# Kernel tuning notes

Hardware: AMD Instinct MI355X
Metric: run time of the kernel (lower is better)

## Reference

```python
import jax, jax.numpy as jnp
import numpy as np

NUM_EMBEDDINGS = 4096
EMBEDDING_DIM = 256
COMMITMENT_COST = 0.25
DECAY = 0.99
EPS = 1e-5
NORM_EPS = 1e-6
B, T = 64, 1024


def _l2norm(x):
    # torch.nn.functional.normalize: x / max(||x||_2, eps)
    n = jnp.sqrt(jnp.sum(x * x, axis=-1, keepdims=True))
    return x / jnp.maximum(n, NORM_EPS)


def setup_inputs() -> dict:
    key = jax.random.key(0)
    k1, k2 = jax.random.split(key)
    z = jax.random.normal(k1, (B, EMBEDDING_DIM, T), dtype=jnp.float32)
    weight = jax.random.normal(k2, (NUM_EMBEDDINGS, EMBEDDING_DIM), dtype=jnp.float32)
    weight = weight.at[0].set(0.0)  # reserved zero code
    ema_cluster_size = jnp.zeros((NUM_EMBEDDINGS,), dtype=jnp.float32)
    ema_w = weight  # buffer initialized as a clone of the codebook
    return {"z": z, "weight": weight, "ema_cluster_size": ema_cluster_size, "ema_w": ema_w}


def reference(z, weight, ema_cluster_size, ema_w):
    K = weight.shape[0]
    zp = jnp.transpose(z, (0, 2, 1))            # [B, T, D]
    b, t, d = zp.shape
    flat_z = zp.reshape(-1, d)                  # [N, D]
    flat_z_norm = _l2norm(flat_z)
    weight_norm = _l2norm(weight)
    # cosine similarity; argmin(1 - cos) == argmax(cos); code 0 excluded via -inf
    cos_sim = jnp.einsum('nd,kd->nk', flat_z_norm, weight_norm)
    cos_sim = cos_sim.at[:, 0].set(-jnp.inf)
    idx = jnp.argmax(cos_sim, axis=1)           # [N] int
    q = weight[idx].reshape(zp.shape)           # [B, T, D]

    # --- training-mode EMA codebook update (buffer math, no grad) ---
    counts = jax.ops.segment_sum(jnp.ones_like(idx, dtype=flat_z.dtype), idx, num_segments=K)
    new_cs = DECAY * ema_cluster_size + (1.0 - DECAY) * counts
    dw = jax.ops.segment_sum(flat_z_norm, idx, num_segments=K)  # [K, D]
    new_ema_w = DECAY * ema_w + (1.0 - DECAY) * dw
    new_cs = new_cs.at[0].set(0.0)
    new_ema_w = new_ema_w.at[0].set(0.0)
    n = jnp.sum(new_cs)
    cluster_size = (new_cs + EPS) / (n + K * EPS) * n
    new_weight = _l2norm(new_ema_w / cluster_size[:, None])
    new_weight = new_weight.at[0].set(0.0)

    loss = COMMITMENT_COST * jnp.mean((jax.lax.stop_gradient(q) - zp) ** 2)
    quantized = zp + jax.lax.stop_gradient(q - zp)  # straight-through
    quantized = jnp.transpose(quantized, (0, 2, 1))  # back to [B, D, T]
    codes = idx.reshape(b, t)
    return quantized, loss, codes, new_weight, new_cs, new_ema_w
```

## Files before the change

kernel.cpp:

```cpp
#include <hip/hip_runtime.h>
#include <math.h>

#define NUM_K 4096
#define DIM   256
#define TLEN  1024
#define DT    (DIM * TLEN)
#define CAP   2048

typedef short bf16x8 __attribute__((ext_vector_type(8)));
typedef float f32x4  __attribute__((ext_vector_type(4)));

static __device__ __forceinline__ unsigned short f2bf(float x) {
  unsigned u = __float_as_uint(x);
  u += 0x7fffu + ((u >> 16) & 1u);
  return (unsigned short)(u >> 16);
}

static __device__ __forceinline__ f32x4 mfma16(bf16x8 a, bf16x8 b, f32x4 c) {
  return __builtin_amdgcn_mfma_f32_16x16x32_bf16(a, b, c, 0, 0, 0);
}

__global__ __launch_bounds__(256) void wnorm_kernel(const float* __restrict__ w,
                                                    float* __restrict__ wnorms) {
  const int k = blockIdx.x * 256 + threadIdx.x;
  const float* row = w + (size_t)k * DIM;
  float p[2];
#pragma unroll
  for (int blk = 0; blk < 2; ++blk) {
    const float* b = row + blk * 128;
    float r[8];
#pragma unroll
    for (int j = 0; j < 8; ++j) r[j] = __fmul_rn(b[j], b[j]);
    for (int i = 8; i < 128; i += 8) {
#pragma unroll
      for (int j = 0; j < 8; ++j) r[j] = __fadd_rn(r[j], __fmul_rn(b[i + j], b[i + j]));
    }
    p[blk] = __fadd_rn(__fadd_rn(__fadd_rn(r[0], r[1]), __fadd_rn(r[2], r[3])),
                       __fadd_rn(__fadd_rn(r[4], r[5]), __fadd_rn(r[6], r[7])));
  }
  wnorms[k] = fmaxf(__fsqrt_rn(__fadd_rn(p[0], p[1])), 1e-6f);
}

__global__ __launch_bounds__(256) void wfrag_kernel(const float* __restrict__ w,
                                                    const float* __restrict__ wnorms,
                                                    unsigned short* __restrict__ img) {
  const int t = blockIdx.x * 256 + threadIdx.x;
  const int lane = t & 63;
  const int fragid = t >> 6;
  const int jg = fragid & 3;
  const int kb = (fragid >> 2) & 7;
  const int chunk = fragid >> 5;
  const int c  = (chunk << 6) + (jg << 4) + (lane & 15);
  const int d0 = (kb << 5) + ((lane >> 4) << 3);
  const float m = wnorms[c];
  const float* src = w + (size_t)c * DIM + d0;
  union { bf16x8 v; unsigned short u[8]; } o;
#pragma unroll
  for (int u = 0; u < 8; ++u) o.u[u] = f2bf(__fdiv_rn(src[u], m));
  *reinterpret_cast<bf16x8*>(img + (size_t)fragid * 512 + lane * 8) = o.v;
}

__global__ __launch_bounds__(256, 3) void vq_main_kernel(
    const float* __restrict__ z, const float* __restrict__ weight,
    const unsigned short* __restrict__ wimg, const float* __restrict__ wnorms,
    float* __restrict__ znT, float* __restrict__ out_codes,
    float* __restrict__ counts, float* __restrict__ loss_accum) {
  __shared__ float tnorm[64];
  __shared__ float v1p[2][64];
  __shared__ float thr[64];
  __shared__ int   fidx[64];
  __shared__ int   clist[CAP];
  __shared__ float cscore[CAP];
  __shared__ int   ccount;

  const int tid  = threadIdx.x;
  const int bb   = blockIdx.x >> 4;
  const int t0   = (blockIdx.x & 15) << 6;
  const int lane = tid & 63;
  const int wv   = tid >> 6;
  const int wr   = wv >> 1;
  const int wc   = wv & 1;
  const float* zb = z + (size_t)bb * DT + t0;

  bf16x8 afr[2][8];
  {
    const int tloc = (wr << 5) + (lane & 15);
    const int dr   = (lane >> 4) << 3;
#pragma unroll
    for (int i = 0; i < 2; ++i) {
      const float* zc = zb + tloc + (i << 4);
#pragma unroll
      for (int kb = 0; kb < 8; ++kb) {
        union { bf16x8 v; unsigned short u[8]; } a;
#pragma unroll
        for (int u = 0; u < 8; ++u)
          a.u[u] = f2bf(zc[(size_t)((kb << 5) + dr + u) * TLEN]);
        afr[i][kb] = a.v;
      }
    }
  }

  if (tid < 64) {
    const float* zc = zb + tid;
    float p[2];
#pragma unroll
    for (int blk = 0; blk < 2; ++blk) {
      float r[8];
#pragma unroll
      for (int j = 0; j < 8; ++j) {
        const float v = zc[(size_t)(blk * 128 + j) * TLEN];
        r[j] = __fmul_rn(v, v);
      }
      for (int i = 8; i < 128; i += 8) {
#pragma unroll
        for (int j = 0; j < 8; ++j) {
          const float v = zc[(size_t)(blk * 128 + i + j) * TLEN];
          r[j] = __fadd_rn(r[j], __fmul_rn(v, v));
        }
      }
      p[blk] = __fadd_rn(__fadd_rn(__fadd_rn(r[0], r[1]), __fadd_rn(r[2], r[3])),
                         __fadd_rn(__fadd_rn(r[4], r[5]), __fadd_rn(r[6], r[7])));
    }
    tnorm[tid] = fmaxf(__fsqrt_rn(__fadd_rn(p[0], p[1])), 1e-6f);
  }
  if (tid == 0) ccount = 0;

  const unsigned short* bbase = wimg + (wc << 10) + (lane << 3);
  const f32x4 zero4 = {0.f, 0.f, 0.f, 0.f};

  float v1loc[2][4];
#pragma unroll
  for (int i = 0; i < 2; ++i)
#pragma unroll
    for (int r = 0; r < 4; ++r) v1loc[i][r] = -INFINITY;
  {
    const bool lc0 = (wc == 0) && ((lane & 15) == 0);
#pragma unroll 1
    for (int chunk = 0; chunk < 64; ++chunk) {
      const unsigned short* bc_ = bbase + ((size_t)chunk << 14);
      bf16x8 bf[16];
#pragma unroll
      for (int kb = 0; kb < 8; ++kb) {
        bf[kb]     = *reinterpret_cast<const bf16x8*>(bc_ + (kb << 11));
        bf[kb + 8] = *reinterpret_cast<const bf16x8*>(bc_ + (kb << 11) + 512);
      }
      f32x4 acc[2][2];
      acc[0][0] = zero4; acc[0][1] = zero4; acc[1][0] = zero4; acc[1][1] = zero4;
      __builtin_amdgcn_s_setprio(1);
#pragma unroll
      for (int kb = 0; kb < 8; ++kb) {
        acc[0][0] = mfma16(afr[0][kb], bf[kb],     acc[0][0]);
        acc[1][0] = mfma16(afr[1][kb], bf[kb],     acc[1][0]);
        acc[0][1] = mfma16(afr[0][kb], bf[kb + 8], acc[0][1]);
        acc[1][1] = mfma16(afr[1][kb], bf[kb + 8], acc[1][1]);
      }
      __builtin_amdgcn_s_setprio(0);
#pragma unroll
      for (int i = 0; i < 2; ++i)
#pragma unroll
        for (int r = 0; r < 4; ++r) {
          float v0 = acc[i][0][r];
          if (chunk == 0 && lc0) v0 = -INFINITY;
          v1loc[i][r] = fmaxf(v1loc[i][r], fmaxf(v0, acc[i][1][r]));
        }
    }
  }
#pragma unroll
  for (int i = 0; i < 2; ++i)
#pragma unroll
    for (int r = 0; r < 4; ++r) {
      float v = v1loc[i][r];
      v = fmaxf(v, __shfl_xor(v, 1));
      v = fmaxf(v, __shfl_xor(v, 2));
      v = fmaxf(v, __shfl_xor(v, 4));
      v = fmaxf(v, __shfl_xor(v, 8));
      if ((lane & 15) == 0)
        v1p[wc][(wr << 5) + (i << 4) + ((lane >> 4) << 2) + r] = v;
    }
  __syncthreads();
  if (tid < 64) thr[tid] = fmaxf(v1p[0][tid], v1p[1][tid]) - 0.02f * tnorm[tid];
  __syncthreads();

  float thrv_[2][4];
  {
    const int tb = (wr << 5) + ((lane >> 4) << 2);
#pragma unroll
    for (int i = 0; i < 2; ++i)
#pragma unroll
      for (int r = 0; r < 4; ++r) thrv_[i][r] = thr[tb + (i << 4) + r];
  }

  {
#pragma unroll 1
    for (int chunk = 0; chunk < 64; ++chunk) {
      const unsigned short* bc_ = bbase + ((size_t)chunk << 14);
      bf16x8 bf[16];
#pragma unroll
      for (int kb = 0; kb < 8; ++kb) {
        bf[kb]     = *reinterpret_cast<const bf16x8*>(bc_ + (kb << 11));
        bf[kb + 8] = *reinterpret_cast<const bf16x8*>(bc_ + (kb << 11) + 512);
      }
      f32x4 acc[2][2];
      acc[0][0] = zero4; acc[0][1] = zero4; acc[1][0] = zero4; acc[1][1] = zero4;
      __builtin_amdgcn_s_setprio(1);
#pragma unroll
      for (int kb = 0; kb < 8; ++kb) {
        acc[0][0] = mfma16(afr[0][kb], bf[kb],     acc[0][0]);
        acc[1][0] = mfma16(afr[1][kb], bf[kb],     acc[1][0]);
        acc[0][1] = mfma16(afr[0][kb], bf[kb + 8], acc[0][1]);
        acc[1][1] = mfma16(afr[1][kb], bf[kb + 8], acc[1][1]);
      }
      __builtin_amdgcn_s_setprio(0);
#pragma unroll
      for (int i = 0; i < 2; ++i)
#pragma unroll
        for (int j = 0; j < 2; ++j) {
          const int c = (chunk << 6) + (wc << 5) + (j << 4) + (lane & 15);
#pragma unroll
          for (int r = 0; r < 4; ++r) {
            if (acc[i][j][r] >= thrv_[i][r] && c != 0) {
              const int pos = atomicAdd(&ccount, 1);
              if (pos < CAP)
                clist[pos] = (c << 7) | ((wr << 5) + (i << 4) + ((lane >> 4) << 2) + r);
            }
          }
        }
    }
  }
  __syncthreads();

  const int ncand = min(ccount, CAP);
  for (int e = tid; e < ncand; e += 256) {
    const int pk = clist[e];
    const int tloc = pk & 127;
    const int c = pk >> 7;
    const float m  = tnorm[tloc];
    const float mc = wnorms[c];
    const float* zc = zb + tloc;
    const float* wp = weight + (size_t)c * DIM;
    float s = 0.f;
#pragma unroll 8
    for (int d = 0; d < DIM; ++d)
      s = fmaf(__fdiv_rn(zc[(size_t)d * TLEN], m), __fdiv_rn(wp[d], mc), s);
    cscore[e] = s;
  }
  __syncthreads();

  if (tid < 64) {
    float best = -INFINITY; int bc = NUM_K;
    for (int e = 0; e < ncand; ++e) {
      const int pk = clist[e];
      if ((pk & 127) == tid) {
        const float s = cscore[e]; const int c = pk >> 7;
        if (s > best || (s == best && c < bc)) { best = s; bc = c; }
      }
    }
    if (bc >= NUM_K) bc = 1;
    fidx[tid] = bc;
    out_codes[bb * TLEN + t0 + tid] = (float)bc;
    atomicAdd(&counts[bc], 1.0f);
  }
  __syncthreads();

  {
    const int gbase = (bb << 10) + t0;
    float lpart = 0.f;
#pragma unroll 4
    for (int r = 0; r < 16; ++r) {
      const int tk = (r << 2) + wv;
      const int code = fidx[tk];
      const float m = tnorm[tk];
      const float* zc = zb + tk;
      const float4 w4 = *reinterpret_cast<const float4*>(
          weight + (size_t)code * DIM + (lane << 2));
      float4 zr4;
      zr4.x = zc[(size_t)((lane << 2) + 0) * TLEN];
      zr4.y = zc[(size_t)((lane << 2) + 1) * TLEN];
      zr4.z = zc[(size_t)((lane << 2) + 2) * TLEN];
      zr4.w = zc[(size_t)((lane << 2) + 3) * TLEN];
      float4 zn4;
      zn4.x = __fdiv_rn(zr4.x, m);
      zn4.y = __fdiv_rn(zr4.y, m);
      zn4.z = __fdiv_rn(zr4.z, m);
      zn4.w = __fdiv_rn(zr4.w, m);
      *reinterpret_cast<float4*>(znT + (size_t)(gbase + tk) * DIM + (lane << 2)) = zn4;
      const float dx = w4.x - zr4.x, dy = w4.y - zr4.y;
      const float dz = w4.z - zr4.z, dw_ = w4.w - zr4.w;
      lpart = fmaf(dx, dx, lpart); lpart = fmaf(dy, dy, lpart);
      lpart = fmaf(dz, dz, lpart); lpart = fmaf(dw_, dw_, lpart);
    }
#pragma unroll
    for (int off = 32; off; off >>= 1) lpart += __shfl_down(lpart, off, 64);
    if (lane == 0) atomicAdd(loss_accum, lpart);
  }
}

__global__ __launch_bounds__(256) void finalize_cs_kernel(
    const float* __restrict__ counts, const float* __restrict__ ema_cs,
    float* __restrict__ out_ncs, float* __restrict__ ws_n,
    const float* __restrict__ loss_accum, float* __restrict__ out_loss,
    int* __restrict__ offsets) {
  __shared__ float redf[4];
  __shared__ int   redi[4];
  const int tid = threadIdx.x;
  const int lane = tid & 63, wv = tid >> 6;
  const int base = tid << 4;
  int cloc[16]; int csum = 0; float fsum = 0.f;
#pragma unroll
  for (int j = 0; j < 16; ++j) {
    const int k = base + j;
    const float cf = counts[k];
    const float v = (k == 0) ? 0.f : 0.99f * ema_cs[k] + 0.01f * cf;
    out_ncs[k] = v; fsum += v;
    cloc[j] = csum; csum += (int)cf;
  }
  int inc = csum;
#pragma unroll
  for (int off = 1; off < 64; off <<= 1) {
    const int t = __shfl_up(inc, off, 64);
    if (lane >= off) inc += t;
  }
  float fs = fsum;
#pragma unroll
  for (int off = 32; off; off >>= 1) fs += __shfl_down(fs, off, 64);
  if (lane == 63) redi[wv] = inc;
  if (lane == 0)  redf[wv] = fs;
  __syncthreads();
  int wbase = 0;
#pragma unroll
  for (int w = 0; w < 4; ++w) wbase += (w < wv) ? redi[w] : 0;
  const int tbase = wbase + inc - csum;
#pragma unroll
  for (int j = 0; j < 16; ++j) offsets[base + j] = tbase + cloc[j];
  if (tid == 0) {
    ws_n[0] = redf[0] + redf[1] + redf[2] + redf[3];
    out_loss[0] = 0.25f * loss_accum[0] / 16777216.0f;
  }
}

__global__ __launch_bounds__(256) void scatter_kernel(
    const float* __restrict__ codes, const int* __restrict__ offsets,
    int* __restrict__ cursor, int* __restrict__ bucket) {
  const int g = blockIdx.x * 256 + threadIdx.x;
  const int c = (int)codes[g];
  const int pos = atomicAdd(&cursor[c], 1);
  bucket[offsets[c] + pos] = g;
}

__global__ __launch_bounds__(256) void dw_kernel(
    const float* __restrict__ znT, const float* __restrict__ counts,
    const int* __restrict__ offsets, const int* __restrict__ bucket,
    float* __restrict__ dw) {
  const int c = blockIdx.x;
  const int cnt = (int)counts[c];
  const int off = offsets[c];
  const int tid = threadIdx.x;
  float acc = 0.f;
  for (int i = 0; i < cnt; ++i) {
    const int g = bucket[off + i];
    acc += znT[(size_t)g * DIM + tid];
  }
  dw[(size_t)c * DIM + tid] = acc;
}

__global__ __launch_bounds__(256) void finalize_w_kernel(
    const float* __restrict__ ema_w, const float* __restrict__ ncs,
    const float* __restrict__ ws_n, float* __restrict__ new_ema_w,
    float* __restrict__ new_weight) {
  const int wid  = threadIdx.x >> 6;
  const int lane = threadIdx.x & 63;
  const int k    = (blockIdx.x << 2) + wid;
  const float n  = ws_n[0];
  const float cs = (ncs[k] + 1e-5f) / (n + 4096.0f * 1e-5f) * n;
  const float* erow = ema_w + k * DIM;
  float* nrow = new_ema_w + k * DIM;
  float* wrow = new_weight + k * DIM;
  const int d0 = lane << 2;
  float u[4]; float ss = 0.f;
#pragma unroll
  for (int j = 0; j < 4; ++j) {
    const float dwv = nrow[d0 + j];
    const float val = (k == 0) ? 0.f : 0.99f * erow[d0 + j] + 0.01f * dwv;
    nrow[d0 + j] = val;
    const float uu = val / cs;
    u[j] = uu;
    ss = fmaf(uu, uu, ss);
  }
#pragma unroll
  for (int off = 32; off; off >>= 1) ss += __shfl_xor(ss, off, 64);
  const float m = fmaxf(sqrtf(ss), 1e-6f);
#pragma unroll
  for (int j = 0; j < 4; ++j) wrow[d0 + j] = u[j] / m;
}

__global__ __launch_bounds__(256) void qwrite_kernel(
    const float* __restrict__ codes, const float* __restrict__ weight,
    float* __restrict__ out_q) {
  const int bb = blockIdx.x >> 4;
  const int t0 = (blockIdx.x & 15) << 6;
  const int ln = threadIdx.x & 63, qv = threadIdx.x >> 6;
  const int code = (int)codes[bb * TLEN + t0 + ln];
  const float* wrow = weight + (size_t)code * DIM;
  float* qb = out_q + (size_t)bb * DT + t0 + ln;
#pragma unroll 4
  for (int dd = 0; dd < 64; ++dd) {
    const int d = (qv << 6) + dd;
    qb[(size_t)d * TLEN] = wrow[d];
  }
}

extern "C" void kernel_launch(void* const* d_in, const int* in_sizes, int n_in,
                              void* d_out, int out_size, void* d_ws, size_t ws_size,
                              hipStream_t stream) {
  const float* z      = (const float*)d_in[0];
  const float* weight = (const float*)d_in[1];
  const float* ema_cs = (const float*)d_in[2];
  const float* ema_w  = (const float*)d_in[3];

  float* out = (float*)d_out;
  float* out_q     = out;
  float* out_loss  = out + 16777216;
  float* out_codes = out + 16777217;
  float* out_nw    = out + 16842753;
  float* out_ncs   = out + 17891329;
  float* out_new   = out + 17895425;

  float* counts     = (float*)d_ws;
  float* loss_accum = counts + 4096;
  float* ws_n       = counts + 4097;
  float* wnorms     = counts + 4352;

  unsigned short* wimg = (unsigned short*)(out_nw + 3);
  int* bucket  = (int*)(out_nw + 3);
  int* offsets = (int*)(out_nw + 524292);
  int* cursor  = (int*)(out_nw + 528388);

  hipMemsetAsync(d_ws, 0, 4098 * sizeof(float), stream);
  hipMemsetAsync(cursor, 0, 4096 * sizeof(int), stream);

  wnorm_kernel<<<16, 256, 0, stream>>>(weight, wnorms);
  wfrag_kernel<<<512, 256, 0, stream>>>(weight, wnorms, wimg);
  vq_main_kernel<<<1024, 256, 0, stream>>>(z, weight, wimg, wnorms, out_q ,
                                           out_codes, counts, loss_accum);
  finalize_cs_kernel<<<1, 256, 0, stream>>>(counts, ema_cs, out_ncs, ws_n,
                                            loss_accum, out_loss, offsets);
  scatter_kernel<<<256, 256, 0, stream>>>(out_codes, offsets, cursor, bucket);
  dw_kernel<<<NUM_K, 256, 0, stream>>>(out_q , counts, offsets, bucket, out_new);
  finalize_w_kernel<<<NUM_K / 4, 256, 0, stream>>>(ema_w, out_ncs, ws_n,
                                                   out_new, out_nw);
  qwrite_kernel<<<1024, 256, 0, stream>>>(out_codes, weight, out_q);
}
```

Before: 864.4 us.

## Double-buffer codebook fragment loads and precompute normalized vectors for rescoring

Both MFMA passes over the codebook now double-buffer the B fragments, loading the next chunk while the current one is multiplied, with sched barriers and a min-occupancy launch bound lowered from 3 to 2 to make room for the extra registers. Normalized z rows are written up front, and a separate kernel writes fp32 normalized codebook rows into the output scratch area. The candidate rescoring loop then reads those precomputed vectors instead of doing strided loads and two divisions per element. The costs are lower occupancy, an extra kernel launch and extra global traffic for the normalized weights.

New measurement: 759.8 us. 12.1% less time.

```diff
diff --git a/kernel.cpp b/kernel.cpp
--- a/kernel.cpp
+++ b/kernel.cpp
@@ -41,8 +41,19 @@
   wnorms[k] = fmaxf(__fsqrt_rn(__fadd_rn(p[0], p[1])), 1e-6f);
 }
 
-__global__ __launch_bounds__(256) void wfrag_kernel(const float* __restrict__ w,
+__global__ __launch_bounds__(256) void wnf32_kernel(const float* __restrict__ w,
                                                     const float* __restrict__ wnorms,
+                                                    float* __restrict__ wnf) {
+  const int idx = blockIdx.x * 256 + threadIdx.x;
+  const float m = wnorms[idx >> 6];
+  const float4 v = *reinterpret_cast<const float4*>(w + (size_t)idx * 4);
+  float4 o;
+  o.x = __fdiv_rn(v.x, m); o.y = __fdiv_rn(v.y, m);
+  o.z = __fdiv_rn(v.z, m); o.w = __fdiv_rn(v.w, m);
+  *reinterpret_cast<float4*>(wnf + (size_t)idx * 4) = o;
+}
+
+__global__ __launch_bounds__(256) void wfrag_kernel(const float* __restrict__ wnf,
                                                     unsigned short* __restrict__ img) {
   const int t = blockIdx.x * 256 + threadIdx.x;
   const int lane = t & 63;
@@ -52,19 +63,19 @@
   const int chunk = fragid >> 5;
   const int c  = (chunk << 6) + (jg << 4) + (lane & 15);
   const int d0 = (kb << 5) + ((lane >> 4) << 3);
-  const float m = wnorms[c];
-  const float* src = w + (size_t)c * DIM + d0;
+  const float* src = wnf + (size_t)c * DIM + d0;
   union { bf16x8 v; unsigned short u[8]; } o;
 #pragma unroll
-  for (int u = 0; u < 8; ++u) o.u[u] = f2bf(__fdiv_rn(src[u], m));
+  for (int u = 0; u < 8; ++u) o.u[u] = f2bf(src[u]);
   *reinterpret_cast<bf16x8*>(img + (size_t)fragid * 512 + lane * 8) = o.v;
 }
 
-__global__ __launch_bounds__(256, 3) void vq_main_kernel(
+__global__ __launch_bounds__(256, 2) void vq_main_kernel(
     const float* __restrict__ z, const float* __restrict__ weight,
-    const unsigned short* __restrict__ wimg, const float* __restrict__ wnorms,
+    const unsigned short* __restrict__ wimg, const float* __restrict__ wnf32,
     float* __restrict__ znT, float* __restrict__ out_codes,
     float* __restrict__ counts, float* __restrict__ loss_accum) {
+  __shared__ float pp[2][64];
   __shared__ float tnorm[64];
   __shared__ float v1p[2][64];
   __shared__ float thr[64];
@@ -82,6 +93,46 @@
   const int wc   = wv & 1;
   const float* zb = z + (size_t)bb * DT + t0;
 
+  if (tid < 128) {
+    const int tok = tid & 63, blk = tid >> 6;
+    const float* zc = zb + tok;
+    float r[8];
+#pragma unroll
+    for (int j = 0; j < 8; ++j) {
+      const float v = zc[(size_t)(blk * 128 + j) * TLEN];
+      r[j] = __fmul_rn(v, v);
+    }
+    for (int i = 8; i < 128; i += 8) {
+#pragma unroll
+      for (int j = 0; j < 8; ++j) {
+        const float v = zc[(size_t)(blk * 128 + i + j) * TLEN];
+        r[j] = __fadd_rn(r[j], __fmul_rn(v, v));
+      }
+    }
+    pp[blk][tok] = __fadd_rn(__fadd_rn(__fadd_rn(r[0], r[1]), __fadd_rn(r[2], r[3])),
+                             __fadd_rn(__fadd_rn(r[4], r[5]), __fadd_rn(r[6], r[7])));
+  }
+  if (tid == 0) ccount = 0;
+  __syncthreads();
+  if (tid < 64) tnorm[tid] = fmaxf(__fsqrt_rn(__fadd_rn(pp[0][tid], pp[1][tid])), 1e-6f);
+  __syncthreads();
+
+  {
+    const int tok = tid & 63, seg = tid >> 6;
+    const float m = tnorm[tok];
+    const float* zc = zb + tok;
+    float* orow = znT + (size_t)((bb << 10) + t0 + tok) * DIM + (seg << 6);
+#pragma unroll 4
+    for (int k4 = 0; k4 < 16; ++k4) {
+      float4 o;
+      o.x = __fdiv_rn(zc[(size_t)((seg << 6) + (k4 << 2) + 0) * TLEN], m);
+      o.y = __fdiv_rn(zc[(size_t)((seg << 6) + (k4 << 2) + 1) * TLEN], m);
+      o.z = __fdiv_rn(zc[(size_t)((seg << 6) + (k4 << 2) + 2) * TLEN], m);
+      o.w = __fdiv_rn(zc[(size_t)((seg << 6) + (k4 << 2) + 3) * TLEN], m);
+      *reinterpret_cast<float4*>(&orow[k4 << 2]) = o;
+    }
+  }
+
   bf16x8 afr[2][8];
   {
     const int tloc = (wr << 5) + (lane & 15);
@@ -100,33 +151,31 @@
     }
   }
 
-  if (tid < 64) {
-    const float* zc = zb + tid;
-    float p[2];
-#pragma unroll
-    for (int blk = 0; blk < 2; ++blk) {
-      float r[8];
-#pragma unroll
-      for (int j = 0; j < 8; ++j) {
-        const float v = zc[(size_t)(blk * 128 + j) * TLEN];
-        r[j] = __fmul_rn(v, v);
-      }
-      for (int i = 8; i < 128; i += 8) {
-#pragma unroll
-        for (int j = 0; j < 8; ++j) {
-          const float v = zc[(size_t)(blk * 128 + i + j) * TLEN];
-          r[j] = __fadd_rn(r[j], __fmul_rn(v, v));
-        }
-      }
-      p[blk] = __fadd_rn(__fadd_rn(__fadd_rn(r[0], r[1]), __fadd_rn(r[2], r[3])),
-                         __fadd_rn(__fadd_rn(r[4], r[5]), __fadd_rn(r[6], r[7])));
-    }
-    tnorm[tid] = fmaxf(__fsqrt_rn(__fadd_rn(p[0], p[1])), 1e-6f);
-  }
-  if (tid == 0) ccount = 0;
-
   const unsigned short* bbase = wimg + (wc << 10) + (lane << 3);
   const f32x4 zero4 = {0.f, 0.f, 0.f, 0.f};
+  const bool lc0 = (wc == 0) && ((lane & 15) == 0);
+
+#define LOADC(buf, ch) do {                                              \
+    const unsigned short* p_ = bbase + ((size_t)(ch) << 14);             \
+    _Pragma("unroll")                                                    \
+    for (int kb_ = 0; kb_ < 8; ++kb_) {                                  \
+      buf[kb_]     = *reinterpret_cast<const bf16x8*>(p_ + (kb_ << 11)); \
+      buf[kb_ + 8] = *reinterpret_cast<const bf16x8*>(p_ + (kb_ << 11) + 512); \
+    }                                                                    \
+    __builtin_amdgcn_sched_barrier(0);                                   \
+  } while (0)
+
+#define MFMAC(buf, accv) do {                                            \
+    __builtin_amdgcn_s_setprio(1);                                       \
+    _Pragma("unroll")                                                    \
+    for (int kb_ = 0; kb_ < 8; ++kb_) {                                  \
+      accv[0][0] = mfma16(afr[0][kb_], buf[kb_],     accv[0][0]);        \
+      accv[1][0] = mfma16(afr[1][kb_], buf[kb_],     accv[1][0]);        \
+      accv[0][1] = mfma16(afr[0][kb_], buf[kb_ + 8], accv[0][1]);        \
+      accv[1][1] = mfma16(afr[1][kb_], buf[kb_ + 8], accv[1][1]);        \
+    }                                                                    \
+    __builtin_amdgcn_s_setprio(0);                                       \
+  } while (0)
 
   float v1loc[2][4];
 #pragma unroll
@@ -134,35 +183,34 @@
 #pragma unroll
     for (int r = 0; r < 4; ++r) v1loc[i][r] = -INFINITY;
   {
-    const bool lc0 = (wc == 0) && ((lane & 15) == 0);
+    bf16x8 bA[16], bB[16];
+    LOADC(bA, 0);
 #pragma unroll 1
-    for (int chunk = 0; chunk < 64; ++chunk) {
-      const unsigned short* bc_ = bbase + ((size_t)chunk << 14);
-      bf16x8 bf[16];
-#pragma unroll
-      for (int kb = 0; kb < 8; ++kb) {
-        bf[kb]     = *reinterpret_cast<const bf16x8*>(bc_ + (kb << 11));
-        bf[kb + 8] = *reinterpret_cast<const bf16x8*>(bc_ + (kb << 11) + 512);
-      }
+    for (int chunk = 0; chunk < 64; chunk += 2) {
+      LOADC(bB, chunk + 1);
       f32x4 acc[2][2];
       acc[0][0] = zero4; acc[0][1] = zero4; acc[1][0] = zero4; acc[1][1] = zero4;
-      __builtin_amdgcn_s_setprio(1);
-#pragma unroll
-      for (int kb = 0; kb < 8; ++kb) {
-        acc[0][0] = mfma16(afr[0][kb], bf[kb],     acc[0][0]);
-        acc[1][0] = mfma16(afr[1][kb], bf[kb],     acc[1][0]);
-        acc[0][1] = mfma16(afr[0][kb], bf[kb + 8], acc[0][1]);
-        acc[1][1] = mfma16(afr[1][kb], bf[kb + 8], acc[1][1]);
+      MFMAC(bA, acc);
+      {
+        const bool m0 = (chunk == 0) && lc0;
+#pragma unroll
+        for (int i = 0; i < 2; ++i)
+#pragma unroll
+          for (int r = 0; r < 4; ++r) {
+            float v0 = acc[i][0][r];
+            if (m0) v0 = -INFINITY;
+            v1loc[i][r] = fmaxf(v1loc[i][r], fmaxf(v0, acc[i][1][r]));
+          }
       }
-      __builtin_amdgcn_s_setprio(0);
+      if (chunk + 2 < 64) LOADC(bA, chunk + 2);
+      f32x4 ac2[2][2];
+      ac2[0][0] = zero4; ac2[0][1] = zero4; ac2[1][0] = zero4; ac2[1][1] = zero4;
+      MFMAC(bB, ac2);
 #pragma unroll
       for (int i = 0; i < 2; ++i)
 #pragma unroll
-        for (int r = 0; r < 4; ++r) {
-          float v0 = acc[i][0][r];
-          if (chunk == 0 && lc0) v0 = -INFINITY;
-          v1loc[i][r] = fmaxf(v1loc[i][r], fmaxf(v0, acc[i][1][r]));
-        }
+        for (int r = 0; r < 4; ++r)
+          v1loc[i][r] = fmaxf(v1loc[i][r], fmaxf(ac2[i][0][r], ac2[i][1][r]));
     }
   }
 #pragma unroll
@@ -191,26 +239,14 @@
   }
 
   {
+    bf16x8 bA[16], bB[16];
+    LOADC(bA, 0);
 #pragma unroll 1
-    for (int chunk = 0; chunk < 64; ++chunk) {
-      const unsigned short* bc_ = bbase + ((size_t)chunk << 14);
-      bf16x8 bf[16];
-#pragma unroll
-      for (int kb = 0; kb < 8; ++kb) {
-        bf[kb]     = *reinterpret_cast<const bf16x8*>(bc_ + (kb << 11));
-        bf[kb + 8] = *reinterpret_cast<const bf16x8*>(bc_ + (kb << 11) + 512);
-      }
+    for (int chunk = 0; chunk < 64; chunk += 2) {
+      LOADC(bB, chunk + 1);
       f32x4 acc[2][2];
       acc[0][0] = zero4; acc[0][1] = zero4; acc[1][0] = zero4; acc[1][1] = zero4;
-      __builtin_amdgcn_s_setprio(1);
-#pragma unroll
-      for (int kb = 0; kb < 8; ++kb) {
-        acc[0][0] = mfma16(afr[0][kb], bf[kb],     acc[0][0]);
-        acc[1][0] = mfma16(afr[1][kb], bf[kb],     acc[1][0]);
-        acc[0][1] = mfma16(afr[0][kb], bf[kb + 8], acc[0][1]);
-        acc[1][1] = mfma16(afr[1][kb], bf[kb + 8], acc[1][1]);
-      }
-      __builtin_amdgcn_s_setprio(0);
+      MFMAC(bA, acc);
 #pragma unroll
       for (int i = 0; i < 2; ++i)
 #pragma unroll
@@ -225,8 +261,28 @@
             }
           }
         }
-    }
-  }
+      if (chunk + 2 < 64) LOADC(bA, chunk + 2);
+      f32x4 ac2[2][2];
+      ac2[0][0] = zero4; ac2[0][1] = zero4; ac2[1][0] = zero4; ac2[1][1] = zero4;
+      MFMAC(bB, ac2);
+#pragma unroll
+      for (int i = 0; i < 2; ++i)
+#pragma unroll
+        for (int j = 0; j < 2; ++j) {
+          const int c = ((chunk + 1) << 6) + (wc << 5) + (j << 4) + (lane & 15);
+#pragma unroll
+          for (int r = 0; r < 4; ++r) {
+            if (ac2[i][j][r] >= thrv_[i][r]) {
+              const int pos = atomicAdd(&ccount, 1);
+              if (pos < CAP)
+                clist[pos] = (c << 7) | ((wr << 5) + (i << 4) + ((lane >> 4) << 2) + r);
+            }
+          }
+        }
+    }
+  }
+#undef LOADC
+#undef MFMAC
   __syncthreads();
 
   const int ncand = min(ccount, CAP);
@@ -234,14 +290,12 @@
     const int pk = clist[e];
     const int tloc = pk & 127;
     const int c = pk >> 7;
-    const float m  = tnorm[tloc];
-    const float mc = wnorms[c];
-    const float* zc = zb + tloc;
-    const float* wp = weight + (size_t)c * DIM;
+    const float* za = znT + (size_t)((bb << 10) + t0 + tloc) * DIM;
+    const float* wa = wnf32 + (size_t)c * DIM;
     float s = 0.f;
 #pragma unroll 8
     for (int d = 0; d < DIM; ++d)
-      s = fmaf(__fdiv_rn(zc[(size_t)d * TLEN], m), __fdiv_rn(wp[d], mc), s);
+      s = fmaf(za[d], wa[d], s);
     cscore[e] = s;
   }
   __syncthreads();
@@ -263,13 +317,11 @@
   __syncthreads();
 
   {
-    const int gbase = (bb << 10) + t0;
     float lpart = 0.f;
 #pragma unroll 4
     for (int r = 0; r < 16; ++r) {
       const int tk = (r << 2) + wv;
       const int code = fidx[tk];
-      const float m = tnorm[tk];
       const float* zc = zb + tk;
       const float4 w4 = *reinterpret_cast<const float4*>(
           weight + (size_t)code * DIM + (lane << 2));
@@ -278,12 +330,6 @@
       zr4.y = zc[(size_t)((lane << 2) + 1) * TLEN];
       zr4.z = zc[(size_t)((lane << 2) + 2) * TLEN];
       zr4.w = zc[(size_t)((lane << 2) + 3) * TLEN];
-      float4 zn4;
-      zn4.x = __fdiv_rn(zr4.x, m);
-      zn4.y = __fdiv_rn(zr4.y, m);
-      zn4.z = __fdiv_rn(zr4.z, m);
-      zn4.w = __fdiv_rn(zr4.w, m);
-      *reinterpret_cast<float4*>(znT + (size_t)(gbase + tk) * DIM + (lane << 2)) = zn4;
       const float dx = w4.x - zr4.x, dy = w4.y - zr4.y;
       const float dz = w4.z - zr4.z, dw_ = w4.w - zr4.w;
       lpart = fmaf(dx, dx, lpart); lpart = fmaf(dy, dy, lpart);
@@ -434,13 +480,15 @@
   int* bucket  = (int*)(out_nw + 3);
   int* offsets = (int*)(out_nw + 524292);
   int* cursor  = (int*)(out_nw + 528388);
+  float* wnf32 = out_new;
 
   hipMemsetAsync(d_ws, 0, 4098 * sizeof(float), stream);
   hipMemsetAsync(cursor, 0, 4096 * sizeof(int), stream);
 
   wnorm_kernel<<<16, 256, 0, stream>>>(weight, wnorms);
-  wfrag_kernel<<<512, 256, 0, stream>>>(weight, wnorms, wimg);
-  vq_main_kernel<<<1024, 256, 0, stream>>>(z, weight, wimg, wnorms, out_q ,
+  wnf32_kernel<<<1024, 256, 0, stream>>>(weight, wnorms, wnf32);
+  wfrag_kernel<<<512, 256, 0, stream>>>(wnf32, wimg);
+  vq_main_kernel<<<1024, 256, 0, stream>>>(z, weight, wimg, wnf32, out_q ,
                                            out_codes, counts, loss_accum);
   finalize_cs_kernel<<<1, 256, 0, stream>>>(counts, ema_cs, out_ncs, ws_n,
                                             loss_accum, out_loss, offsets);
```
